# Kernel optimization log

Hardware: AMD Instinct MI355X
Metric: run time of the kernel (lower is better)

## Reference

```python
import jax, jax.numpy as jnp
import numpy as np

N_NODES, N_EDGES = 50000, 800000
IN_DIM, HID_DIM, OUT_DIM = 512, 256, 256


def setup_inputs() -> dict:
    key = jax.random.key(0)
    ks = jax.random.split(key, 8)
    x = jax.random.normal(ks[0], (N_NODES, IN_DIM), dtype=jnp.float32)
    edge_index = jax.random.randint(ks[1], (2, N_EDGES), 0, N_NODES, dtype=jnp.int64)
    # GCNConv lin weights (no bias in lin; separate additive bias after aggregation)
    W1 = jax.random.normal(ks[2], (IN_DIM, HID_DIM), dtype=jnp.float32) * (1.0 / np.sqrt(IN_DIM))
    b1 = jnp.zeros((HID_DIM,), dtype=jnp.float32)
    W2 = jax.random.normal(ks[3], (HID_DIM, OUT_DIM), dtype=jnp.float32) * (1.0 / np.sqrt(HID_DIM))
    b2 = jnp.zeros((OUT_DIM,), dtype=jnp.float32)
    # projection head nn.Linear(out_dim, out_dim)
    Wp = jax.random.normal(ks[4], (OUT_DIM, OUT_DIM), dtype=jnp.float32) * (1.0 / np.sqrt(OUT_DIM))
    bp = jnp.zeros((OUT_DIM,), dtype=jnp.float32)
    return {"x": x, "edge_index": edge_index, "W1": W1, "b1": b1,
            "W2": W2, "b2": b2, "Wp": Wp, "bp": bp}


def _gcn_conv(x, W, b, src, dst, n):
    # x' = D^{-1/2}(A+I)D^{-1/2} (x W) + b ; deg includes self-loop (+1)
    h = x @ W  # [N, F]
    deg = jax.ops.segment_sum(jnp.ones(src.shape[0], h.dtype), dst, num_segments=n) + 1.0
    dis = jax.lax.rsqrt(deg)  # deg^{-1/2}, [N]
    msg = (dis[src] * dis[dst])[:, None] * h[src]  # [E, F] gathered+scaled messages
    agg = jax.ops.segment_sum(msg, dst, num_segments=n)  # scatter-add to dst
    # self-loop contribution: norm = dis[i]^2, message = h[i]
    return agg + (dis * dis)[:, None] * h + b


def reference(x, edge_index, W1, b1, W2, b2, Wp, bp):
    src, dst = edge_index[0], edge_index[1]
    n = x.shape[0]
    h = jax.nn.relu(_gcn_conv(x, W1, b1, src, dst, n))
    # eval mode: dropout is identity
    h = _gcn_conv(h, W2, b2, src, dst, n)
    return h @ Wp + bp
```

## Files before the change

### kernel.cpp

```cpp
#include <hip/hip_runtime.h>
#include <hip/hip_bf16.h>

typedef __bf16 bf16_8 __attribute__((ext_vector_type(8)));
typedef float  f32_4  __attribute__((ext_vector_type(4)));

#define NNODES 50000
#define NEDGES 800000
#define INDIM  512
#define HIDDIM 256
#define LDS_STRIDE 264

__device__ inline void gload_lds16(const __hip_bfloat16* g, __hip_bfloat16* l) {
    __builtin_amdgcn_global_load_lds(
        (const __attribute__((address_space(1))) void*)g,
        (__attribute__((address_space(3))) void*)l, 16, 0, 0);
}


__global__ void zero_kernel(int* p, int n) {
    int i = blockIdx.x * 256 + threadIdx.x;
    if (i < n) p[i] = 0;
}

__global__ void detect_kernel(const int* __restrict__ ei,
                              const unsigned short* __restrict__ xh,
                              int* __restrict__ flags) {
    int t = threadIdx.x;
    unsigned long long nz = __ballot(ei[1 + 2 * t] != 0);
    unsigned e = (xh[2 * t] >> 7) & 0xFF;
    unsigned long long ok = __ballot(e >= 90 && e <= 142);
    if (t == 0) {
        flags[0] = (nz == 0ull) ? 1 : 0;
        flags[1] = (__popcll(ok) >= 48) ? 1 : 0;
    }
}

__global__ void count_kernel(const int* __restrict__ idx, const int* __restrict__ flags,
                             int* __restrict__ deg, int E) {
    int e = blockIdx.x * 256 + threadIdx.x;
    if (e >= E) return;
    int d = flags[0] ? idx[2 * (E + e)] : idx[E + e];
    d = min(max(d, 0), NNODES - 1);
    atomicAdd(&deg[d], 1);
}

__global__ void reduce_kernel(const int* __restrict__ deg, int* __restrict__ bsum, int n) {
    __shared__ int l[256];
    int i = blockIdx.x * 256 + threadIdx.x;
    l[threadIdx.x] = (i < n) ? deg[i] : 0;
    __syncthreads();
    for (int o = 128; o > 0; o >>= 1) {
        if (threadIdx.x < o) l[threadIdx.x] += l[threadIdx.x + o];
        __syncthreads();
    }
    if (threadIdx.x == 0) bsum[blockIdx.x] = l[0];
}

__global__ void scanb_kernel(const int* __restrict__ bsum, int nb,
                             int* __restrict__ boff, int* __restrict__ offs_last) {
    __shared__ int l[256];
    int v = (threadIdx.x < nb) ? bsum[threadIdx.x] : 0;
    l[threadIdx.x] = v;
    __syncthreads();
    for (int o = 1; o < 256; o <<= 1) {
        int t = (threadIdx.x >= o) ? l[threadIdx.x - o] : 0;
        __syncthreads();
        l[threadIdx.x] += t;
        __syncthreads();
    }
    if (threadIdx.x < nb) boff[threadIdx.x] = l[threadIdx.x] - v;
    if (threadIdx.x == 255) *offs_last = l[255];
}

__global__ void local_scan_kernel(const int* __restrict__ deg, const int* __restrict__ boff,
                                  int* __restrict__ offs, float* __restrict__ dis, int n) {
    __shared__ int l[256];
    int i = blockIdx.x * 256 + threadIdx.x;
    int v = (i < n) ? deg[i] : 0;
    l[threadIdx.x] = v;
    __syncthreads();
    for (int o = 1; o < 256; o <<= 1) {
        int t = (threadIdx.x >= o) ? l[threadIdx.x - o] : 0;
        __syncthreads();
        l[threadIdx.x] += t;
        __syncthreads();
    }
    if (i < n) {
        offs[i] = boff[blockIdx.x] + l[threadIdx.x] - v;
        dis[i]  = rsqrtf((float)v + 1.0f);
    }
}

__global__ void fill_kernel(const int* __restrict__ idx, const int* __restrict__ flags,
                            const int* __restrict__ offs, int* __restrict__ cursor,
                            int* __restrict__ csr, int E) {
    int e = blockIdx.x * 256 + threadIdx.x;
    if (e >= E) return;
    int s, d;
    if (flags[0]) { s = idx[2 * e]; d = idx[2 * (E + e)]; }
    else          { s = idx[e];     d = idx[E + e]; }
    s = min(max(s, 0), NNODES - 1);
    d = min(max(d, 0), NNODES - 1);
    int p = atomicAdd(&cursor[d], 1);
    csr[offs[d] + p] = s;
}

__global__ void repack_kernel(const void* __restrict__ Wv, const int* __restrict__ flags,
                              __hip_bfloat16* __restrict__ P, int K, int N) {
    int ntiles = N / 16;
    int nt = blockIdx.x % ntiles;
    int kt = blockIdx.x / ntiles;
    int lane = threadIdx.x;
    int quad = lane >> 4, l16 = lane & 15;
    size_t pbase = ((size_t)blockIdx.x * 64 + lane) * 8;
    int k0 = kt * 32 + quad * 8;
    int col = nt * 16 + l16;
    bool bf = flags[1] != 0;
    for (int j = 0; j < 8; ++j) {
        size_t src = (size_t)(k0 + j) * N + col;
        P[pbase + j] = bf ? ((const __hip_bfloat16*)Wv)[src]
                          : (__hip_bfloat16)((const float*)Wv)[src];
    }
}

template<int K>
__global__ __launch_bounds__(256, 4)
void gemm_kernel(const void* __restrict__ Av,
                 const __hip_bfloat16* __restrict__ Bp,
                 const void* __restrict__ biasv,
                 void* __restrict__ Cv,
                 const int* __restrict__ flags, int amode, int cmode,
                 int M) {
    constexpr int N = 256;
    __shared__ __align__(16) __hip_bfloat16 smem[64 * LDS_STRIDE];
    const int wave = threadIdx.x >> 6;
    const int lane = threadIdx.x & 63;
    const int quad = lane >> 4;
    const int l16  = lane & 15;
    const int rowblock = blockIdx.x * 64;
    const int rowbase  = rowblock + wave * 16;
    const bool active  = rowbase < M;
    const bool bf  = flags[1] != 0;
    const bool abf = amode || bf;
    const bool cbf = cmode || bf;

    f32_4 acc[16] = {};

    const size_t arowbase = active ? ((size_t)(rowbase + l16) * K + quad * 8) : 0;

    #pragma unroll
    for (int kb = 0; kb < K / 64; ++kb) {
        bf16_8 a[2];
        if (active) {
            #pragma unroll
            for (int t = 0; t < 2; ++t) {
                size_t ab = arowbase + (size_t)(kb * 64 + t * 32);
                if (abf) {
                    a[t] = *(const bf16_8*)((const __hip_bfloat16*)Av + ab);
                } else {
                    const float* Af = (const float*)Av + ab;
                    f32_4 lo = *(const f32_4*)Af;
                    f32_4 hi = *(const f32_4*)(Af + 4);
                    #pragma unroll
                    for (int j = 0; j < 4; ++j) { a[t][j] = (__bf16)lo[j]; a[t][j + 4] = (__bf16)hi[j]; }
                }
            }
        }
        __syncthreads();
        const __hip_bfloat16* slab = Bp + (size_t)kb * 16384;
        #pragma unroll
        for (int i = 0; i < 8; ++i) {
            int c = wave * 8 + i;
            gload_lds16(slab + c * 512 + lane * 8, smem + c * 512);
        }
        __syncthreads();
        if (active) {
            #pragma unroll
            for (int t = 0; t < 2; ++t) {
                const __hip_bfloat16* bbase = smem + t * 8192 + lane * 8;
                #pragma unroll
                for (int ct = 0; ct < 16; ++ct) {
                    bf16_8 b = *(const bf16_8*)(bbase + ct * 512);
                    acc[ct] = __builtin_amdgcn_mfma_f32_16x16x32_bf16(a[t], b, acc[ct], 0, 0, 0);
                }
            }
        }
    }

    __syncthreads();
    if (cbf) {
        if (active) {
            #pragma unroll
            for (int ct = 0; ct < 16; ++ct) {
                int col = ct * 16 + l16;
                float bv = 0.0f;
                if (biasv) bv = bf ? (float)((const __hip_bfloat16*)biasv)[col]
                                   : ((const float*)biasv)[col];
                #pragma unroll
                for (int rr = 0; rr < 4; ++rr) {
                    int rloc = wave * 16 + quad * 4 + rr;
                    smem[rloc * LDS_STRIDE + col] = (__hip_bfloat16)(acc[ct][rr] + bv);
                }
            }
        }
        __syncthreads();
        int t = threadIdx.x;
        int r = t >> 2, q = t & 3;
        if (rowblock + r < M) {
            __hip_bfloat16* crow = (__hip_bfloat16*)Cv + (size_t)(rowblock + r) * N;
            #pragma unroll
            for (int j = 0; j < 8; ++j) {
                int col = q * 64 + j * 8;
                bf16_8 v = *(const bf16_8*)(smem + r * LDS_STRIDE + col);
                *(bf16_8*)(crow + col) = v;
            }
        }
    } else if (active) {
        #pragma unroll
        for (int ct = 0; ct < 16; ++ct) {
            int col = ct * 16 + l16;
            float bv = 0.0f;
            if (biasv) bv = bf ? (float)((const __hip_bfloat16*)biasv)[col]
                               : ((const float*)biasv)[col];
            #pragma unroll
            for (int rr = 0; rr < 4; ++rr) {
                int row = rowbase + quad * 4 + rr;
                ((float*)Cv)[(size_t)row * N + col] = acc[ct][rr] + bv;
            }
        }
    }
}

__device__ inline void acc_row(f32_4& a0, f32_4& a1, float w, bf16_8 r) {
    a0[0] += w * (float)r[0]; a0[1] += w * (float)r[1];
    a0[2] += w * (float)r[2]; a0[3] += w * (float)r[3];
    a1[0] += w * (float)r[4]; a1[1] += w * (float)r[5];
    a1[2] += w * (float)r[6]; a1[3] += w * (float)r[7];
}

__global__ __launch_bounds__(256)
void agg_kernel(const __hip_bfloat16* __restrict__ h,
                const int* __restrict__ csr,
                const int* __restrict__ offs,
                const float* __restrict__ dis,
                const void* __restrict__ biasv,
                const int* __restrict__ flags,
                __hip_bfloat16* __restrict__ out,
                int relu) {
    const int wave = threadIdx.x >> 6;
    const int lane = threadIdx.x & 63;
    const int n = blockIdx.x * 4 + wave;
    if (n >= NNODES) return;
    const int half = lane >> 5;
    const int l32  = lane & 31;

    const float dn = dis[n];
    const int beg = offs[n], end = offs[n + 1];
    f32_4 a0 = {}, a1 = {};

    int j = beg + half;
    for (; j + 2 < end; j += 4) {
        int sa = csr[j], sb = csr[j + 2];
        bf16_8 ra = *(const bf16_8*)(h + (size_t)sa * HIDDIM + l32 * 8);
        bf16_8 rb = *(const bf16_8*)(h + (size_t)sb * HIDDIM + l32 * 8);
        float wa = dis[sa], wb = dis[sb];
        acc_row(a0, a1, wa, ra);
        acc_row(a0, a1, wb, rb);
    }
    if (j < end) {
        int sa = csr[j];
        bf16_8 ra = *(const bf16_8*)(h + (size_t)sa * HIDDIM + l32 * 8);
        acc_row(a0, a1, dis[sa], ra);
    }

    #pragma unroll
    for (int k = 0; k < 4; ++k) {
        a0[k] += __shfl_xor(a0[k], 32);
        a1[k] += __shfl_xor(a1[k], 32);
    }

    bf16_8 rn = *(const bf16_8*)(h + (size_t)n * HIDDIM + l32 * 8);
    float bv[8];
    if (flags[1]) {
        bf16_8 bb = ((const bf16_8*)biasv)[l32];
        #pragma unroll
        for (int k = 0; k < 8; ++k) bv[k] = (float)bb[k];
    } else {
        f32_4 blo = *((const f32_4*)biasv + 2 * l32);
        f32_4 bhi = *((const f32_4*)biasv + 2 * l32 + 1);
        #pragma unroll
        for (int k = 0; k < 4; ++k) { bv[k] = blo[k]; bv[k + 4] = bhi[k]; }
    }
    const float dn2 = dn * dn;
    float v[8];
    #pragma unroll
    for (int k = 0; k < 4; ++k) {
        v[k]     = dn * a0[k] + dn2 * (float)rn[k]     + bv[k];
        v[k + 4] = dn * a1[k] + dn2 * (float)rn[k + 4] + bv[k + 4];
    }
    if (relu) {
        #pragma unroll
        for (int k = 0; k < 8; ++k) v[k] = fmaxf(v[k], 0.0f);
    }
    if (half == 0) {
        bf16_8 o;
        #pragma unroll
        for (int k = 0; k < 8; ++k) o[k] = (__bf16)v[k];
        *(bf16_8*)(out + (size_t)n * HIDDIM + l32 * 8) = o;
    }
}


extern "C" void kernel_launch(void* const* d_in, const int* in_sizes, int n_in,
                              void* d_out, int out_size, void* d_ws, size_t ws_size,
                              hipStream_t stream) {
    const int M = NNODES, E = NEDGES;
    const void* x  = d_in[0];
    const int*  ei = (const int*)d_in[1];
    const void* W1 = d_in[2];
    const void* b1 = d_in[3];
    const void* W2 = d_in[4];
    const void* b2 = d_in[5];
    const void* Wp = d_in[6];
    const void* bp = d_in[7];

    char* w = (char*)d_ws;
    size_t off = 0;
    auto alloc = [&](size_t bytes) -> void* {
        void* p = w + off;
        off += (bytes + 255) & ~(size_t)255;
        return p;
    };
    int*   deg    = (int*)alloc((size_t)M * 4);
    int*   cursor = (int*)alloc((size_t)M * 4);
    int*   offs   = (int*)alloc((size_t)(M + 1) * 4);
    float* dis    = (float*)alloc((size_t)M * 4);
    int*   flags  = (int*)alloc(256);
    int*   bsum   = (int*)alloc(256 * 4);
    int*   boff   = (int*)alloc(256 * 4);
    int*   csr    = (int*)alloc((size_t)E * 4);
    __hip_bfloat16* W1p = (__hip_bfloat16*)alloc((size_t)INDIM * HIDDIM * 2);
    __hip_bfloat16* W2p = (__hip_bfloat16*)alloc((size_t)HIDDIM * HIDDIM * 2);
    __hip_bfloat16* Wpp = (__hip_bfloat16*)alloc((size_t)HIDDIM * HIDDIM * 2);
    if (ws_size < off) return;

    __hip_bfloat16* h  = (__hip_bfloat16*)d_out;
    __hip_bfloat16* ha = (__hip_bfloat16*)d_in[0];

    const int nb = (M + 255) / 256;

    zero_kernel<<<nb, 256, 0, stream>>>(deg, M);
    zero_kernel<<<nb, 256, 0, stream>>>(cursor, M);
    detect_kernel<<<1, 64, 0, stream>>>(ei, (const unsigned short*)x, flags);
    count_kernel<<<(E + 255) / 256, 256, 0, stream>>>(ei, flags, deg, E);
    reduce_kernel<<<nb, 256, 0, stream>>>(deg, bsum, M);
    scanb_kernel<<<1, 256, 0, stream>>>(bsum, nb, boff, &offs[M]);
    local_scan_kernel<<<nb, 256, 0, stream>>>(deg, boff, offs, dis, M);
    fill_kernel<<<(E + 255) / 256, 256, 0, stream>>>(ei, flags, offs, cursor, csr, E);

    repack_kernel<<<(INDIM / 32) * (HIDDIM / 16), 64, 0, stream>>>(W1, flags, W1p, INDIM, HIDDIM);
    repack_kernel<<<(HIDDIM / 32) * (HIDDIM / 16), 64, 0, stream>>>(W2, flags, W2p, HIDDIM, HIDDIM);
    repack_kernel<<<(HIDDIM / 32) * (HIDDIM / 16), 64, 0, stream>>>(Wp, flags, Wpp, HIDDIM, HIDDIM);

    const int ggrid = (M + 63) / 64;
    const int agrid = (M + 3) / 4;

    gemm_kernel<INDIM><<<ggrid, 256, 0, stream>>>(x, W1p, nullptr, h, flags, 0, 1, M);
    agg_kernel<<<agrid, 256, 0, stream>>>(h, csr, offs, dis, b1, flags, ha, 1);

    gemm_kernel<HIDDIM><<<ggrid, 256, 0, stream>>>(ha, W2p, nullptr, h, flags, 1, 1, M);
    agg_kernel<<<agrid, 256, 0, stream>>>(h, csr, offs, dis, b2, flags, ha, 0);

    gemm_kernel<HIDDIM><<<ggrid, 256, 0, stream>>>(ha, Wpp, bp, d_out, flags, 1, 0, M);
}
```

Measured before the change: 463.5 us.

## Fold W2 and projection into one weight, aggregate before GEMM, double-buffer GEMM B tiles

Precomputes Wf = W2·Wp and a fused bias b2·Wp + bp in a small kernel. The second layer then aggregates the hidden features first, since aggregation is linear, and applies a single GEMM with Wf. This drops one full N×256×256 GEMM pass and its memory traffic. The GEMM main loop is also restructured into a double-buffered LDS pipeline with explicit waitcnt and barriers, and a register ring for A prefetch. In exchange, the product W2·Wp is rounded to bf16, which changes the numerics.

Result: slower. 505.0 us (+8.9%).

```diff
diff --git a/kernel.cpp b/kernel.cpp
--- a/kernel.cpp
+++ b/kernel.cpp
@@ -8,7 +8,7 @@
 #define NEDGES 800000
 #define INDIM  512
 #define HIDDIM 256
-#define LDS_STRIDE 264
+#define CSTRIDE 264
 
 __device__ inline void gload_lds16(const __hip_bfloat16* g, __hip_bfloat16* l) {
     __builtin_amdgcn_global_load_lds(
@@ -103,6 +103,34 @@
     d = min(max(d, 0), NNODES - 1);
     int p = atomicAdd(&cursor[d], 1);
     csr[offs[d] + p] = s;
+}
+
+__global__ void wf_kernel(const void* __restrict__ W2v, const void* __restrict__ Wpv,
+                          const void* __restrict__ b2v, const void* __restrict__ bpv,
+                          const int* __restrict__ flags,
+                          void* __restrict__ Wfv, void* __restrict__ bfv) {
+    const bool bf = flags[1] != 0;
+    const int r = blockIdx.x;
+    const int c = threadIdx.x;
+    float acc = 0.0f;
+    for (int k = 0; k < HIDDIM; ++k) {
+        float a = (r < HIDDIM)
+            ? (bf ? (float)((const __hip_bfloat16*)W2v)[(size_t)r * HIDDIM + k]
+                  : ((const float*)W2v)[(size_t)r * HIDDIM + k])
+            : (bf ? (float)((const __hip_bfloat16*)b2v)[k]
+                  : ((const float*)b2v)[k]);
+        float b = bf ? (float)((const __hip_bfloat16*)Wpv)[(size_t)k * HIDDIM + c]
+                     : ((const float*)Wpv)[(size_t)k * HIDDIM + c];
+        acc += a * b;
+    }
+    if (r < HIDDIM) {
+        if (bf) ((__hip_bfloat16*)Wfv)[(size_t)r * HIDDIM + c] = (__hip_bfloat16)acc;
+        else    ((float*)Wfv)[(size_t)r * HIDDIM + c] = acc;
+    } else {
+        acc += bf ? (float)((const __hip_bfloat16*)bpv)[c] : ((const float*)bpv)[c];
+        if (bf) ((__hip_bfloat16*)bfv)[c] = (__hip_bfloat16)acc;
+        else    ((float*)bfv)[c] = acc;
+    }
 }
 
 __global__ void repack_kernel(const void* __restrict__ Wv, const int* __restrict__ flags,
@@ -123,72 +151,107 @@
     }
 }
 
+template<int K, bool ABF>
+__device__ __forceinline__ void gemm_loop(const void* __restrict__ Av,
+                                          const __hip_bfloat16* __restrict__ Bp,
+                                          __hip_bfloat16* smem, f32_4 (&acc)[16],
+                                          int wave, int lane, int row0, bool active) {
+    constexpr int NKB = K / 32;
+    const int quad = lane >> 4;
+    const int l16  = lane & 15;
+    __hip_bfloat16* buf0 = smem;
+    __hip_bfloat16* buf1 = smem + 8192;
+    const size_t arowK = (size_t)(active ? row0 + l16 : l16) * K;
+
+    bf16_8 afr[3];
+
+    auto stage = [&](int s) {
+        const __hip_bfloat16* slab = Bp + (size_t)s * 8192;
+        __hip_bfloat16* buf = (s & 1) ? buf1 : buf0;
+        #pragma unroll
+        for (int i = 0; i < 4; ++i) {
+            int ch = wave * 4 + i;
+            gload_lds16(slab + ch * 512 + lane * 8, buf + ch * 512);
+        }
+    };
+    auto loadA = [&](int s) -> bf16_8 {
+        return *(const bf16_8*)((const __hip_bfloat16*)Av + arowK + (size_t)s * 32 + quad * 8);
+    };
+    auto loadA32 = [&](int s) -> bf16_8 {
+        const float* Af = (const float*)Av + arowK + (size_t)s * 32 + quad * 8;
+        f32_4 lo = *(const f32_4*)Af;
+        f32_4 hi = *(const f32_4*)(Af + 4);
+        bf16_8 r;
+        #pragma unroll
+        for (int j = 0; j < 4; ++j) { r[j] = (__bf16)lo[j]; r[j + 4] = (__bf16)hi[j]; }
+        return r;
+    };
+
+    if constexpr (ABF) afr[0] = loadA(0);
+    stage(0);
+    if constexpr (ABF) afr[1] = loadA(1);
+    stage(1);
+
+    #pragma unroll
+    for (int s = 0; s < NKB; ++s) {
+        if (s + 1 < NKB) {
+            if constexpr (ABF) asm volatile("s_waitcnt vmcnt(5)" ::: "memory");
+            else               asm volatile("s_waitcnt vmcnt(4)" ::: "memory");
+        } else {
+            asm volatile("s_waitcnt vmcnt(0)" ::: "memory");
+        }
+        __builtin_amdgcn_sched_barrier(0);
+        __builtin_amdgcn_s_barrier();
+        __builtin_amdgcn_sched_barrier(0);
+        if (ABF && s + 2 < NKB) afr[(s + 2) % 3] = loadA(s + 2);
+        bf16_8 a;
+        if constexpr (ABF) a = afr[s % 3];
+        else               a = loadA32(s);
+        if (active) {
+            const __hip_bfloat16* bb = ((s & 1) ? buf1 : buf0) + lane * 8;
+            #pragma unroll
+            for (int ct = 0; ct < 16; ++ct) {
+                bf16_8 b = *(const bf16_8*)(bb + ct * 512);
+                acc[ct] = __builtin_amdgcn_mfma_f32_16x16x32_bf16(a, b, acc[ct], 0, 0, 0);
+            }
+        }
+        __builtin_amdgcn_sched_barrier(0);
+        asm volatile("s_waitcnt lgkmcnt(0)" ::: "memory");
+        __builtin_amdgcn_sched_barrier(0);
+        __builtin_amdgcn_s_barrier();
+        __builtin_amdgcn_sched_barrier(0);
+        if (s + 2 < NKB) stage(s + 2);
+    }
+}
+
 template<int K>
 __global__ __launch_bounds__(256, 4)
 void gemm_kernel(const void* __restrict__ Av,
+                 const void* __restrict__ Av_alt,
                  const __hip_bfloat16* __restrict__ Bp,
                  const void* __restrict__ biasv,
                  void* __restrict__ Cv,
-                 const int* __restrict__ flags, int amode, int cmode,
-                 int M) {
+                 const int* __restrict__ flags, int amode, int cmode, int M) {
     constexpr int N = 256;
-    __shared__ __align__(16) __hip_bfloat16 smem[64 * LDS_STRIDE];
+    __shared__ __align__(16) __hip_bfloat16 smem[16896];
+
     const int wave = threadIdx.x >> 6;
     const int lane = threadIdx.x & 63;
     const int quad = lane >> 4;
     const int l16  = lane & 15;
-    const int rowblock = blockIdx.x * 64;
-    const int rowbase  = rowblock + wave * 16;
-    const bool active  = rowbase < M;
+    const int row0 = blockIdx.x * 64 + wave * 16;
+    const bool active = row0 < M;
     const bool bf  = flags[1] != 0;
     const bool abf = amode || bf;
     const bool cbf = cmode || bf;
+    const void* A = (bf || !Av_alt) ? Av : Av_alt;
 
     f32_4 acc[16] = {};
-
-    const size_t arowbase = active ? ((size_t)(rowbase + l16) * K + quad * 8) : 0;
-
-    #pragma unroll
-    for (int kb = 0; kb < K / 64; ++kb) {
-        bf16_8 a[2];
-        if (active) {
-            #pragma unroll
-            for (int t = 0; t < 2; ++t) {
-                size_t ab = arowbase + (size_t)(kb * 64 + t * 32);
-                if (abf) {
-                    a[t] = *(const bf16_8*)((const __hip_bfloat16*)Av + ab);
-                } else {
-                    const float* Af = (const float*)Av + ab;
-                    f32_4 lo = *(const f32_4*)Af;
-                    f32_4 hi = *(const f32_4*)(Af + 4);
-                    #pragma unroll
-                    for (int j = 0; j < 4; ++j) { a[t][j] = (__bf16)lo[j]; a[t][j + 4] = (__bf16)hi[j]; }
-                }
-            }
-        }
-        __syncthreads();
-        const __hip_bfloat16* slab = Bp + (size_t)kb * 16384;
-        #pragma unroll
-        for (int i = 0; i < 8; ++i) {
-            int c = wave * 8 + i;
-            gload_lds16(slab + c * 512 + lane * 8, smem + c * 512);
-        }
-        __syncthreads();
-        if (active) {
-            #pragma unroll
-            for (int t = 0; t < 2; ++t) {
-                const __hip_bfloat16* bbase = smem + t * 8192 + lane * 8;
-                #pragma unroll
-                for (int ct = 0; ct < 16; ++ct) {
-                    bf16_8 b = *(const bf16_8*)(bbase + ct * 512);
-                    acc[ct] = __builtin_amdgcn_mfma_f32_16x16x32_bf16(a[t], b, acc[ct], 0, 0, 0);
-                }
-            }
-        }
-    }
-
-    __syncthreads();
+    if (abf) gemm_loop<K, true >(A, Bp, smem, acc, wave, lane, row0, active);
+    else     gemm_loop<K, false>(A, Bp, smem, acc, wave, lane, row0, active);
+
     if (cbf) {
+        __hip_bfloat16* cs = smem + wave * 16 * CSTRIDE;
         if (active) {
             #pragma unroll
             for (int ct = 0; ct < 16; ++ct) {
@@ -197,22 +260,16 @@
                 if (biasv) bv = bf ? (float)((const __hip_bfloat16*)biasv)[col]
                                    : ((const float*)biasv)[col];
                 #pragma unroll
-                for (int rr = 0; rr < 4; ++rr) {
-                    int rloc = wave * 16 + quad * 4 + rr;
-                    smem[rloc * LDS_STRIDE + col] = (__hip_bfloat16)(acc[ct][rr] + bv);
-                }
+                for (int rr = 0; rr < 4; ++rr)
+                    cs[(quad * 4 + rr) * CSTRIDE + col] = (__hip_bfloat16)(acc[ct][rr] + bv);
             }
-        }
-        __syncthreads();
-        int t = threadIdx.x;
-        int r = t >> 2, q = t & 3;
-        if (rowblock + r < M) {
-            __hip_bfloat16* crow = (__hip_bfloat16*)Cv + (size_t)(rowblock + r) * N;
-            #pragma unroll
-            for (int j = 0; j < 8; ++j) {
-                int col = q * 64 + j * 8;
-                bf16_8 v = *(const bf16_8*)(smem + r * LDS_STRIDE + col);
-                *(bf16_8*)(crow + col) = v;
+            const int rh = lane >> 5;
+            const int ce = (lane & 31) * 8;
+            #pragma unroll
+            for (int pass = 0; pass < 8; ++pass) {
+                int r = pass * 2 + rh;
+                __hip_bfloat16* crow = (__hip_bfloat16*)Cv + (size_t)(row0 + r) * N;
+                *(bf16_8*)(crow + ce) = *(const bf16_8*)(cs + r * CSTRIDE + ce);
             }
         }
     } else if (active) {
@@ -224,7 +281,7 @@
                                : ((const float*)biasv)[col];
             #pragma unroll
             for (int rr = 0; rr < 4; ++rr) {
-                int row = rowbase + quad * 4 + rr;
+                int row = row0 + quad * 4 + rr;
                 ((float*)Cv)[(size_t)row * N + col] = acc[ct][rr] + bv;
             }
         }
@@ -246,6 +303,7 @@
                 const void* __restrict__ biasv,
                 const int* __restrict__ flags,
                 __hip_bfloat16* __restrict__ out,
+                __hip_bfloat16* __restrict__ out_alt,
                 int relu) {
     const int wave = threadIdx.x >> 6;
     const int lane = threadIdx.x & 63;
@@ -253,6 +311,7 @@
     if (n >= NNODES) return;
     const int half = lane >> 5;
     const int l32  = lane & 31;
+    __hip_bfloat16* o = (flags[1] || !out_alt) ? out : out_alt;
 
     const float dn = dis[n];
     const int beg = offs[n], end = offs[n + 1];
@@ -280,16 +339,18 @@
     }
 
     bf16_8 rn = *(const bf16_8*)(h + (size_t)n * HIDDIM + l32 * 8);
-    float bv[8];
-    if (flags[1]) {
-        bf16_8 bb = ((const bf16_8*)biasv)[l32];
-        #pragma unroll
-        for (int k = 0; k < 8; ++k) bv[k] = (float)bb[k];
-    } else {
-        f32_4 blo = *((const f32_4*)biasv + 2 * l32);
-        f32_4 bhi = *((const f32_4*)biasv + 2 * l32 + 1);
-        #pragma unroll
-        for (int k = 0; k < 4; ++k) { bv[k] = blo[k]; bv[k + 4] = bhi[k]; }
+    float bv[8] = {0, 0, 0, 0, 0, 0, 0, 0};
+    if (biasv) {
+        if (flags[1]) {
+            bf16_8 bb = ((const bf16_8*)biasv)[l32];
+            #pragma unroll
+            for (int k = 0; k < 8; ++k) bv[k] = (float)bb[k];
+        } else {
+            f32_4 blo = *((const f32_4*)biasv + 2 * l32);
+            f32_4 bhi = *((const f32_4*)biasv + 2 * l32 + 1);
+            #pragma unroll
+            for (int k = 0; k < 4; ++k) { bv[k] = blo[k]; bv[k + 4] = bhi[k]; }
+        }
     }
     const float dn2 = dn * dn;
     float v[8];
@@ -303,10 +364,10 @@
         for (int k = 0; k < 8; ++k) v[k] = fmaxf(v[k], 0.0f);
     }
     if (half == 0) {
-        bf16_8 o;
+        bf16_8 ov;
         #pragma unroll
-        for (int k = 0; k < 8; ++k) o[k] = (__bf16)v[k];
-        *(bf16_8*)(out + (size_t)n * HIDDIM + l32 * 8) = o;
+        for (int k = 0; k < 8; ++k) ov[k] = (__bf16)v[k];
+        *(bf16_8*)(o + (size_t)n * HIDDIM + l32 * 8) = ov;
     }
 }
 
@@ -340,12 +401,14 @@
     int*   boff   = (int*)alloc(256 * 4);
     int*   csr    = (int*)alloc((size_t)E * 4);
     __hip_bfloat16* W1p = (__hip_bfloat16*)alloc((size_t)INDIM * HIDDIM * 2);
-    __hip_bfloat16* W2p = (__hip_bfloat16*)alloc((size_t)HIDDIM * HIDDIM * 2);
-    __hip_bfloat16* Wpp = (__hip_bfloat16*)alloc((size_t)HIDDIM * HIDDIM * 2);
+    __hip_bfloat16* Wfp = (__hip_bfloat16*)alloc((size_t)HIDDIM * HIDDIM * 2);
+    void* Wf  = alloc((size_t)HIDDIM * HIDDIM * 4);
+    void* bfu = alloc((size_t)HIDDIM * 4);
     if (ws_size < off) return;
 
     __hip_bfloat16* h  = (__hip_bfloat16*)d_out;
     __hip_bfloat16* ha = (__hip_bfloat16*)d_in[0];
+    __hip_bfloat16* g_alt = (__hip_bfloat16*)((char*)d_in[0] + (size_t)M * INDIM * 4 / 2);
 
     const int nb = (M + 255) / 256;
 
@@ -358,18 +421,16 @@
     local_scan_kernel<<<nb, 256, 0, stream>>>(deg, boff, offs, dis, M);
     fill_kernel<<<(E + 255) / 256, 256, 0, stream>>>(ei, flags, offs, cursor, csr, E);
 
+    wf_kernel<<<HIDDIM + 1, HIDDIM, 0, stream>>>(W2, Wp, b2, bp, flags, Wf, bfu);
     repack_kernel<<<(INDIM / 32) * (HIDDIM / 16), 64, 0, stream>>>(W1, flags, W1p, INDIM, HIDDIM);
-    repack_kernel<<<(HIDDIM / 32) * (HIDDIM / 16), 64, 0, stream>>>(W2, flags, W2p, HIDDIM, HIDDIM);
-    repack_kernel<<<(HIDDIM / 32) * (HIDDIM / 16), 64, 0, stream>>>(Wp, flags, Wpp, HIDDIM, HIDDIM);
+    repack_kernel<<<(HIDDIM / 32) * (HIDDIM / 16), 64, 0, stream>>>(Wf, flags, Wfp, HIDDIM, HIDDIM);
 
     const int ggrid = (M + 63) / 64;
     const int agrid = (M + 3) / 4;
 
-    gemm_kernel<INDIM><<<ggrid, 256, 0, stream>>>(x, W1p, nullptr, h, flags, 0, 1, M);
-    agg_kernel<<<agrid, 256, 0, stream>>>(h, csr, offs, dis, b1, flags, ha, 1);
-
-    gemm_kernel<HIDDIM><<<ggrid, 256, 0, stream>>>(ha, W2p, nullptr, h, flags, 1, 1, M);
-    agg_kernel<<<agrid, 256, 0, stream>>>(h, csr, offs, dis, b2, flags, ha, 0);
-
-    gemm_kernel<HIDDIM><<<ggrid, 256, 0, stream>>>(ha, Wpp, bp, d_out, flags, 1, 0, M);
-}
+    gemm_kernel<INDIM><<<ggrid, 256, 0, stream>>>(x, nullptr, W1p, nullptr, h, flags, 0, 1, M);
+    agg_kernel<<<agrid, 256, 0, stream>>>(h, csr, offs, dis, b1, flags, ha, nullptr, 1);
+
+    agg_kernel<<<agrid, 256, 0, stream>>>(ha, csr, offs, dis, nullptr, flags, h, g_alt, 0);
+    gemm_kernel<HIDDIM><<<ggrid, 256, 0, stream>>>(h, g_alt, Wfp, bfu, d_out, flags, 1, 0, M);
+}
```
